# Optimization experiments

Hardware: AMD Instinct MI355X
Metric: run time of the kernel (lower is better)

Reference implementation:

```python
import jax, jax.numpy as jnp
import numpy as np

B, S, D, H, KD = 4, 2048, 640, 10, 64


def setup_inputs() -> dict:
    key = jax.random.key(0)
    k0, k1, k2, k3, k4 = jax.random.split(key, 5)
    x = jax.random.normal(k0, (B, S, D), dtype=jnp.float32)
    # per-head projection weights, stacked over heads: [H, D, KD]
    Wq = jax.random.normal(k1, (H, D, KD), dtype=jnp.float32) * 0.05
    Wk = jax.random.normal(k2, (H, D, KD), dtype=jnp.float32) * 0.05
    Wv = jax.random.normal(k3, (H, D, KD), dtype=jnp.float32) * 0.05
    # output projection: [H*KD, D]
    Wo = jax.random.normal(k4, (H * KD, D), dtype=jnp.float32) * 0.05
    return {"x": x, "Wq": Wq, "Wk": Wk, "Wv": Wv, "Wo": Wo}


def reference(x, Wq, Wk, Wv, Wo):
    # Batched equivalent of the per-head Python loop:
    # each head computes q=x@Wq_h, k=x@Wk_h, v=x@Wv_h, softmax(q k^T / sqrt(KD)) @ v
    q = jnp.einsum("bsd,hdk->bhsk", x, Wq)
    k = jnp.einsum("bsd,hdk->bhsk", x, Wk)
    v = jnp.einsum("bsd,hdk->bhsk", x, Wv)
    scale = 1.0 / jnp.sqrt(jnp.asarray(KD, x.dtype))
    scores = jnp.einsum("bhsk,bhtk->bhst", q, k) * scale  # [B,H,S,S]
    attn = jax.nn.softmax(scores, axis=-1)
    z = jnp.einsum("bhst,bhtk->bhsk", attn, v)  # [B,H,S,KD]
    # concat heads along last axis (head 0 first, matching the loop order)
    z = z.transpose(0, 2, 1, 3).reshape(x.shape[0], x.shape[1], H * KD)
    return jnp.einsum("bsf,fd->bsd", z, Wo)
```

## Files before the change

kernel.cpp:

```cpp
#include <hip/hip_runtime.h>
#include <hip/hip_bf16.h>

#define B_  4
#define S_  2048
#define D_  640
#define H_  10
#define KD_ 64

typedef __attribute__((ext_vector_type(8))) short  short8;
typedef __attribute__((ext_vector_type(4))) short  short4v;
typedef __attribute__((ext_vector_type(4))) float  floatx4;
typedef __attribute__((ext_vector_type(2))) unsigned int uint2v;

static __device__ __forceinline__ short f2bf(float f) {
    union { __hip_bfloat16 h; short s; } u;
    u.h = __float2bfloat16(f);
    return u.s;
}
static __device__ __forceinline__ unsigned int pack2bf(float a, float b) {
    return (unsigned int)(unsigned short)f2bf(a) |
           ((unsigned int)(unsigned short)f2bf(b) << 16);
}

static __device__ __forceinline__ void gload_lds16(const void* gp, void* lp) {
    __builtin_amdgcn_global_load_lds(
        (const __attribute__((address_space(1))) unsigned int*)gp,
        (__attribute__((address_space(3))) unsigned int*)lp, 16, 0, 0);
}

__global__ __launch_bounds__(256) void prep(
        const float* __restrict__ x,
        const float* __restrict__ Wq, const float* __restrict__ Wk,
        const float* __restrict__ Wv, const float* __restrict__ Wo,
        short* __restrict__ xb, short* __restrict__ BigT,
        short* __restrict__ WoT) {
    __shared__ float tile[32][33];
    int bid = blockIdx.x;
    if (bid < 5120) {
        int idx = (bid * 256 + threadIdx.x) * 4;
        float4 v = *(const float4*)(x + idx);
        short4v o;
        o[0] = f2bf(v.x); o[1] = f2bf(v.y); o[2] = f2bf(v.z); o[3] = f2bf(v.w);
        *(short4v*)(xb + idx) = o;
    } else if (bid < 6320) {
        int flat = bid - 5120;
        int bz = flat / 40, rem = flat % 40;
        int by = rem >> 1, bxx = rem & 1;
        int w = bz / 10, h = bz % 10;
        const float* W = ((w == 0) ? Wq : (w == 1) ? Wk : Wv) + h * 640 * 64;
        short* out = BigT + (w * 640 + h * 64) * 640;
        int c0 = bxx * 32;
        int r0 = by * 32;
        int tx = threadIdx.x & 31, ty = threadIdx.x >> 5;
        #pragma unroll
        for (int k = 0; k < 4; ++k)
            tile[ty + 8 * k][tx] = W[(r0 + ty + 8 * k) * 64 + c0 + tx];
        __syncthreads();
        #pragma unroll
        for (int k = 0; k < 4; ++k)
            out[(c0 + ty + 8 * k) * 640 + r0 + tx] = f2bf(tile[tx][ty + 8 * k]);
    } else {
        int flat = bid - 6320;
        int c0 = (flat % 20) * 32;
        int r0 = (flat / 20) * 32;
        int tx = threadIdx.x & 31, ty = threadIdx.x >> 5;
        #pragma unroll
        for (int k = 0; k < 4; ++k)
            tile[ty + 8 * k][tx] = Wo[(r0 + ty + 8 * k) * 640 + c0 + tx];
        __syncthreads();
        #pragma unroll
        for (int k = 0; k < 4; ++k)
            WoT[(c0 + ty + 8 * k) * 640 + r0 + tx] = f2bf(tile[tx][ty + 8 * k]);
    }
}

__global__ __launch_bounds__(256) void qkv_gemm(
        const short* __restrict__ X, const short* __restrict__ BigT,
        short* __restrict__ qb, short* __restrict__ kb, short* __restrict__ vtb) {
    __shared__ __align__(16) short Ab[128][64];
    __shared__ __align__(16) short Bb[128][64];

    int wave = threadIdx.x >> 6;
    int lane = threadIdx.x & 63;
    int lq = lane & 15, quad = lane >> 4;
    int wm = (wave & 1) * 64, wn = (wave >> 1) * 64;
    int tm = blockIdx.x * 128;
    int tn = blockIdx.y * 128;

    int r8 = lane >> 3;
    int sc = ((lane & 7) ^ r8) * 8;
    const short* Asrc = X    + (tm + wave * 32 + r8) * 640 + sc;
    const short* Bsrc = BigT + (tn + wave * 32 + r8) * 640 + sc;

    floatx4 acc[4][4];
    for (int a = 0; a < 4; ++a)
        for (int n = 0; n < 4; ++n)
            acc[a][n] = (floatx4){0.f, 0.f, 0.f, 0.f};

    int swz = lq & 7;
    for (int k0 = 0; k0 < 640; k0 += 64) {
        __syncthreads();
        #pragma unroll
        for (int c = 0; c < 4; ++c) {
            gload_lds16(Asrc + c * 8 * 640 + k0, &Ab[wave * 32 + c * 8][0]);
            gload_lds16(Bsrc + c * 8 * 640 + k0, &Bb[wave * 32 + c * 8][0]);
        }
        __syncthreads();

        #pragma unroll
        for (int ks = 0; ks < 2; ++ks) {
            short8 af[4], bf[4];
            #pragma unroll
            for (int t = 0; t < 4; ++t) {
                af[t] = *(const short8*)(&Ab[wm + t * 16 + lq][((ks * 4 + quad) ^ swz) * 8]);
                bf[t] = *(const short8*)(&Bb[wn + t * 16 + lq][((ks * 4 + quad) ^ swz) * 8]);
            }
            #pragma unroll
            for (int mt = 0; mt < 4; ++mt)
                #pragma unroll
                for (int nt = 0; nt < 4; ++nt)
                    acc[mt][nt] = __builtin_amdgcn_mfma_f32_16x16x32_bf16(
                        af[mt], bf[nt], acc[mt][nt], 0, 0, 0);
        }
    }

    const float qscale = 0.18033688011112042f;
    #pragma unroll
    for (int nt = 0; nt < 4; ++nt) {
        int n_base = tn + wn + nt * 16;
        int w = n_base / 640, rem = n_base % 640;
        int hh = rem / 64, kd = (rem % 64) + lq;
        #pragma unroll
        for (int mt = 0; mt < 4; ++mt) {
            #pragma unroll
            for (int r = 0; r < 4; ++r) {
                int m = tm + wm + mt * 16 + quad * 4 + r;
                int b = m >> 11, s = m & 2047;
                float val = acc[mt][nt][r];
                if (w == 0) {
                    qb[((b * H_ + hh) * S_ + s) * KD_ + kd] = f2bf(val * qscale);
                } else if (w == 1) {
                    kb[((b * H_ + hh) * S_ + s) * KD_ + kd] = f2bf(val);
                } else {
                    vtb[((b * H_ + hh) * KD_ + kd) * S_ + s] = f2bf(val);
                }
            }
        }
    }
}

__global__ __launch_bounds__(256, 3) void attn(
        const short* __restrict__ qb, const short* __restrict__ kbuf,
        const short* __restrict__ vtb, short* __restrict__ zb) {
    __shared__ __align__(16) short Kbuf[2][64][64];
    __shared__ __align__(16) short Vbuf[2][64][64];
    __shared__ __align__(16) short Pbuf[4][2][16][72];

    int wave = threadIdx.x >> 6;
    int lane = threadIdx.x & 63;
    int lq = lane & 15, quad = lane >> 4;

    int bx = blockIdx.x;
    int xcd = bx & 7, slot = bx >> 3;
    int bh = xcd * 5 + (slot >> 4);
    int qt = slot & 15;
    int b = bh / 10, h = bh % 10;
    int q0 = qt * 128;

    const short* qp = qb + (b * H_ + h) * S_ * KD_;
    const short* kp = kbuf + (b * H_ + h) * S_ * KD_;
    const short* vp = vtb + (b * H_ + h) * KD_ * S_;

    int r8 = lane >> 3;
    int g  = (lane & 7) ^ r8;
    const short* kg0 = kp + (wave * 16 + r8) * 64 + g * 8;
    const short* kg1 = kp + (wave * 16 + 8 + r8) * 64 + g * 8;
    const short* vg0 = vp + (wave * 16 + r8) * (long)S_ + g * 8;
    const short* vg1 = vp + (wave * 16 + 8 + r8) * (long)S_ + g * 8;

    short8 qA0, qA1, qB0, qB1;
    {
        int rowA = q0 + wave * 32 + lq;
        qA0 = *(const short8*)(qp + rowA * 64 + quad * 8);
        qA1 = *(const short8*)(qp + rowA * 64 + 32 + quad * 8);
        qB0 = *(const short8*)(qp + (rowA + 16) * 64 + quad * 8);
        qB1 = *(const short8*)(qp + (rowA + 16) * 64 + 32 + quad * 8);
    }

    floatx4 OA[4], OB[4];
    for (int n = 0; n < 4; ++n) {
        OA[n] = (floatx4){0.f, 0.f, 0.f, 0.f};
        OB[n] = (floatx4){0.f, 0.f, 0.f, 0.f};
    }
    float lsA = 0.f, lsB = 0.f;

    gload_lds16(kg0, &Kbuf[0][wave * 16][0]);
    gload_lds16(kg1, &Kbuf[0][wave * 16 + 8][0]);
    gload_lds16(vg0, &Vbuf[0][wave * 16][0]);
    gload_lds16(vg1, &Vbuf[0][wave * 16 + 8][0]);

    int p = 0;
    int sw = lq & 7;

    for (int t0 = 0; t0 < S_; t0 += 64) {
        __syncthreads();

        if (t0 + 64 < S_) {
            int pn = p ^ 1;
            gload_lds16(kg0 + (t0 + 64) * 64, &Kbuf[pn][wave * 16][0]);
            gload_lds16(kg1 + (t0 + 64) * 64, &Kbuf[pn][wave * 16 + 8][0]);
            gload_lds16(vg0 + (t0 + 64),      &Vbuf[pn][wave * 16][0]);
            gload_lds16(vg1 + (t0 + 64),      &Vbuf[pn][wave * 16 + 8][0]);
        }

        const short* Kb = &Kbuf[p][0][0];
        const short* Vb = &Vbuf[p][0][0];

        floatx4 sTA[4], sTB[4];
        #pragma unroll
        for (int kblk = 0; kblk < 4; ++kblk) {
            const short* krow = Kb + (kblk * 16 + lq) * 64;
            short8 bk0 = *(const short8*)(krow + (quad ^ sw) * 8);
            short8 bk1 = *(const short8*)(krow + ((quad + 4) ^ sw) * 8);
            floatx4 zA = (floatx4){0.f, 0.f, 0.f, 0.f};
            zA = __builtin_amdgcn_mfma_f32_16x16x32_bf16(bk0, qA0, zA, 0, 0, 0);
            sTA[kblk] = __builtin_amdgcn_mfma_f32_16x16x32_bf16(bk1, qA1, zA, 0, 0, 0);
            floatx4 zB = (floatx4){0.f, 0.f, 0.f, 0.f};
            zB = __builtin_amdgcn_mfma_f32_16x16x32_bf16(bk0, qB0, zB, 0, 0, 0);
            sTB[kblk] = __builtin_amdgcn_mfma_f32_16x16x32_bf16(bk1, qB1, zB, 0, 0, 0);
        }

        #pragma unroll
        for (int kblk = 0; kblk < 4; ++kblk) {
            float a0 = __builtin_amdgcn_exp2f(sTA[kblk][0]);
            float a1 = __builtin_amdgcn_exp2f(sTA[kblk][1]);
            float a2 = __builtin_amdgcn_exp2f(sTA[kblk][2]);
            float a3 = __builtin_amdgcn_exp2f(sTA[kblk][3]);
            lsA += (a0 + a1) + (a2 + a3);
            uint2v wa; wa[0] = pack2bf(a0, a1); wa[1] = pack2bf(a2, a3);
            *(uint2v*)(&Pbuf[wave][0][lq][kblk * 16 + quad * 4]) = wa;
            float b0 = __builtin_amdgcn_exp2f(sTB[kblk][0]);
            float b1 = __builtin_amdgcn_exp2f(sTB[kblk][1]);
            float b2 = __builtin_amdgcn_exp2f(sTB[kblk][2]);
            float b3 = __builtin_amdgcn_exp2f(sTB[kblk][3]);
            lsB += (b0 + b1) + (b2 + b3);
            uint2v wb; wb[0] = pack2bf(b0, b1); wb[1] = pack2bf(b2, b3);
            *(uint2v*)(&Pbuf[wave][1][lq][kblk * 16 + quad * 4]) = wb;
        }

        #pragma unroll
        for (int ts = 0; ts < 2; ++ts) {
            short8 pfA = *(const short8*)(&Pbuf[wave][0][lq][ts * 32 + quad * 8]);
            short8 pfB = *(const short8*)(&Pbuf[wave][1][lq][ts * 32 + quad * 8]);
            #pragma unroll
            for (int db = 0; db < 4; ++db) {
                const short* vrow = Vb + (db * 16 + lq) * 64;
                short8 bv = *(const short8*)(vrow + ((ts * 4 + quad) ^ sw) * 8);
                OA[db] = __builtin_amdgcn_mfma_f32_16x16x32_bf16(bv, pfA, OA[db], 0, 0, 0);
                OB[db] = __builtin_amdgcn_mfma_f32_16x16x32_bf16(bv, pfB, OB[db], 0, 0, 0);
            }
        }

        p ^= 1;
    }

    lsA += __shfl_xor(lsA, 16);
    lsA += __shfl_xor(lsA, 32);
    lsB += __shfl_xor(lsB, 16);
    lsB += __shfl_xor(lsB, 32);
    float invA = 1.0f / lsA, invB = 1.0f / lsB;

    int sA = q0 + wave * 32 + lq;
    int sB = sA + 16;
    short* zrA = zb + (b * S_ + sA) * 640 + h * 64;
    short* zrB = zb + (b * S_ + sB) * 640 + h * 64;
    #pragma unroll
    for (int db = 0; db < 4; ++db) {
        uint2v za, zv;
        za[0] = pack2bf(OA[db][0] * invA, OA[db][1] * invA);
        za[1] = pack2bf(OA[db][2] * invA, OA[db][3] * invA);
        *(uint2v*)(zrA + db * 16 + quad * 4) = za;
        zv[0] = pack2bf(OB[db][0] * invB, OB[db][1] * invB);
        zv[1] = pack2bf(OB[db][2] * invB, OB[db][3] * invB);
        *(uint2v*)(zrB + db * 16 + quad * 4) = zv;
    }
}

__global__ __launch_bounds__(256) void out_gemm(
        const short* __restrict__ Z, const short* __restrict__ WoT,
        float* __restrict__ out) {
    __shared__ __align__(16) short Ab[128][64];
    __shared__ __align__(16) short Bb[128][64];

    int wave = threadIdx.x >> 6;
    int lane = threadIdx.x & 63;
    int lq = lane & 15, quad = lane >> 4;
    int wm = (wave & 1) * 64, wn = (wave >> 1) * 64;
    int tm = blockIdx.x * 128;
    int tn = blockIdx.y * 128;

    int r8 = lane >> 3;
    int sc = ((lane & 7) ^ r8) * 8;
    const short* Asrc = Z   + (tm + wave * 32 + r8) * 640 + sc;
    const short* Bsrc = WoT + (tn + wave * 32 + r8) * 640 + sc;

    floatx4 acc[4][4];
    for (int a = 0; a < 4; ++a)
        for (int n = 0; n < 4; ++n)
            acc[a][n] = (floatx4){0.f, 0.f, 0.f, 0.f};

    int swz = lq & 7;
    for (int k0 = 0; k0 < 640; k0 += 64) {
        __syncthreads();
        #pragma unroll
        for (int c = 0; c < 4; ++c) {
            gload_lds16(Asrc + c * 8 * 640 + k0, &Ab[wave * 32 + c * 8][0]);
            gload_lds16(Bsrc + c * 8 * 640 + k0, &Bb[wave * 32 + c * 8][0]);
        }
        __syncthreads();

        #pragma unroll
        for (int ks = 0; ks < 2; ++ks) {
            short8 af[4], bf[4];
            #pragma unroll
            for (int t = 0; t < 4; ++t) {
                af[t] = *(const short8*)(&Ab[wm + t * 16 + lq][((ks * 4 + quad) ^ swz) * 8]);
                bf[t] = *(const short8*)(&Bb[wn + t * 16 + lq][((ks * 4 + quad) ^ swz) * 8]);
            }
            #pragma unroll
            for (int mt = 0; mt < 4; ++mt)
                #pragma unroll
                for (int nt = 0; nt < 4; ++nt)
                    acc[mt][nt] = __builtin_amdgcn_mfma_f32_16x16x32_bf16(
                        af[mt], bf[nt], acc[mt][nt], 0, 0, 0);
        }
    }

    #pragma unroll
    for (int mt = 0; mt < 4; ++mt) {
        #pragma unroll
        for (int nt = 0; nt < 4; ++nt) {
            #pragma unroll
            for (int r = 0; r < 4; ++r) {
                int m = tm + wm + mt * 16 + quad * 4 + r;
                out[m * 640 + tn + wn + nt * 16 + lq] = acc[mt][nt][r];
            }
        }
    }
}

extern "C" void kernel_launch(void* const* d_in, const int* in_sizes, int n_in,
                              void* d_out, int out_size, void* d_ws, size_t ws_size,
                              hipStream_t stream) {
    const float* x  = (const float*)d_in[0];
    const float* Wq = (const float*)d_in[1];
    const float* Wk = (const float*)d_in[2];
    const float* Wv = (const float*)d_in[3];
    const float* Wo = (const float*)d_in[4];
    float* out = (float*)d_out;

    char* ws = (char*)d_ws;
    short* BigT = (short*)(ws);
    short* WoT  = (short*)(ws + 2457600);
    short* xb   = (short*)(ws + 3276800);
    short* qb   = (short*)(ws + 13762560);
    short* kb   = (short*)(ws + 24248320);
    short* vtb  = (short*)(ws + 34734080);
    short* zb   = (short*)(ws + 45219840);

    prep<<<dim3(6720), dim3(256), 0, stream>>>(x, Wq, Wk, Wv, Wo, xb, BigT, WoT);
    qkv_gemm<<<dim3(64, 15), dim3(256), 0, stream>>>(xb, BigT, qb, kb, vtb);
    attn<<<dim3(640), dim3(256), 0, stream>>>(qb, kb, vtb, zb);
    out_gemm<<<dim3(64, 5), dim3(256), 0, stream>>>(zb, WoT, out);
}
```

Before: 199.7 us.

## Compute softmax row sums with MFMA, fast bf16 rounding, transposed V store path

The softmax denominator is now accumulated by an extra MFMA that multiplies a vector of bf16 ones by the P fragments, which removes the per-element VALU adds and the final cross-lane shuffles. It also sums the bf16-rounded P values, so the denominator matches the numerator. The library float-to-bf16 conversion is replaced by an inline round-to-nearest-even bit trick, which drops NaN handling. The QKV GEMM splits Q/K blocks from V blocks, and the V branch swaps the MFMA operands so each lane holds consecutive kd values for the transposed V store. The cost is two extra MFMAs per tile in attention and duplicated GEMM code.

```diff
diff --git a/kernel.cpp b/kernel.cpp
--- a/kernel.cpp
+++ b/kernel.cpp
@@ -12,14 +12,16 @@
 typedef __attribute__((ext_vector_type(4))) float  floatx4;
 typedef __attribute__((ext_vector_type(2))) unsigned int uint2v;
 
-static __device__ __forceinline__ short f2bf(float f) {
-    union { __hip_bfloat16 h; short s; } u;
-    u.h = __float2bfloat16(f);
-    return u.s;
+static __device__ __forceinline__ short f2bf_fast(float f) {
+    unsigned int u = __float_as_uint(f);
+    u += 0x7fffu + ((u >> 16) & 1u);
+    return (short)(u >> 16);
 }
 static __device__ __forceinline__ unsigned int pack2bf(float a, float b) {
-    return (unsigned int)(unsigned short)f2bf(a) |
-           ((unsigned int)(unsigned short)f2bf(b) << 16);
+    unsigned int ua = __float_as_uint(a), ub = __float_as_uint(b);
+    ua += 0x7fffu + ((ua >> 16) & 1u);
+    ub += 0x7fffu + ((ub >> 16) & 1u);
+    return (ua >> 16) | (ub & 0xffff0000u);
 }
 
 static __device__ __forceinline__ void gload_lds16(const void* gp, void* lp) {
@@ -39,9 +41,10 @@
     if (bid < 5120) {
         int idx = (bid * 256 + threadIdx.x) * 4;
         float4 v = *(const float4*)(x + idx);
-        short4v o;
-        o[0] = f2bf(v.x); o[1] = f2bf(v.y); o[2] = f2bf(v.z); o[3] = f2bf(v.w);
-        *(short4v*)(xb + idx) = o;
+        uint2v o;
+        o[0] = pack2bf(v.x, v.y);
+        o[1] = pack2bf(v.z, v.w);
+        *(uint2v*)(xb + idx) = o;
     } else if (bid < 6320) {
         int flat = bid - 5120;
         int bz = flat / 40, rem = flat % 40;
@@ -58,7 +61,7 @@
         __syncthreads();
         #pragma unroll
         for (int k = 0; k < 4; ++k)
-            out[(c0 + ty + 8 * k) * 640 + r0 + tx] = f2bf(tile[tx][ty + 8 * k]);
+            out[(c0 + ty + 8 * k) * 640 + r0 + tx] = f2bf_fast(tile[tx][ty + 8 * k]);
     } else {
         int flat = bid - 6320;
         int c0 = (flat % 20) * 32;
@@ -70,7 +73,7 @@
         __syncthreads();
         #pragma unroll
         for (int k = 0; k < 4; ++k)
-            WoT[(c0 + ty + 8 * k) * 640 + r0 + tx] = f2bf(tile[tx][ty + 8 * k]);
+            WoT[(c0 + ty + 8 * k) * 640 + r0 + tx] = f2bf_fast(tile[tx][ty + 8 * k]);
     }
 }
 
@@ -98,51 +101,88 @@
             acc[a][n] = (floatx4){0.f, 0.f, 0.f, 0.f};
 
     int swz = lq & 7;
-    for (int k0 = 0; k0 < 640; k0 += 64) {
-        __syncthreads();
-        #pragma unroll
-        for (int c = 0; c < 4; ++c) {
-            gload_lds16(Asrc + c * 8 * 640 + k0, &Ab[wave * 32 + c * 8][0]);
-            gload_lds16(Bsrc + c * 8 * 640 + k0, &Bb[wave * 32 + c * 8][0]);
-        }
-        __syncthreads();
-
-        #pragma unroll
-        for (int ks = 0; ks < 2; ++ks) {
-            short8 af[4], bf[4];
-            #pragma unroll
-            for (int t = 0; t < 4; ++t) {
-                af[t] = *(const short8*)(&Ab[wm + t * 16 + lq][((ks * 4 + quad) ^ swz) * 8]);
-                bf[t] = *(const short8*)(&Bb[wn + t * 16 + lq][((ks * 4 + quad) ^ swz) * 8]);
-            }
-            #pragma unroll
-            for (int mt = 0; mt < 4; ++mt)
+
+    if (tn < 1280) {
+        for (int k0 = 0; k0 < 640; k0 += 64) {
+            __syncthreads();
+            #pragma unroll
+            for (int c = 0; c < 4; ++c) {
+                gload_lds16(Asrc + c * 8 * 640 + k0, &Ab[wave * 32 + c * 8][0]);
+                gload_lds16(Bsrc + c * 8 * 640 + k0, &Bb[wave * 32 + c * 8][0]);
+            }
+            __syncthreads();
+            #pragma unroll
+            for (int ks = 0; ks < 2; ++ks) {
+                short8 af[4], bf[4];
+                #pragma unroll
+                for (int t = 0; t < 4; ++t) {
+                    af[t] = *(const short8*)(&Ab[wm + t * 16 + lq][((ks * 4 + quad) ^ swz) * 8]);
+                    bf[t] = *(const short8*)(&Bb[wn + t * 16 + lq][((ks * 4 + quad) ^ swz) * 8]);
+                }
+                #pragma unroll
+                for (int mt = 0; mt < 4; ++mt)
+                    #pragma unroll
+                    for (int nt = 0; nt < 4; ++nt)
+                        acc[mt][nt] = __builtin_amdgcn_mfma_f32_16x16x32_bf16(
+                            af[mt], bf[nt], acc[mt][nt], 0, 0, 0);
+            }
+        }
+        const float qscale = 0.18033688011112042f;
+        short* dst = (tn < 640) ? qb : kb;
+        float scale = (tn < 640) ? qscale : 1.0f;
+        #pragma unroll
+        for (int nt = 0; nt < 4; ++nt) {
+            int rem = (tn + wn + nt * 16) % 640;
+            int hh = rem / 64, kd = (rem % 64) + lq;
+            #pragma unroll
+            for (int mt = 0; mt < 4; ++mt) {
+                #pragma unroll
+                for (int r = 0; r < 4; ++r) {
+                    int m = tm + wm + mt * 16 + quad * 4 + r;
+                    int b = m >> 11, s = m & 2047;
+                    dst[((b * H_ + hh) * S_ + s) * KD_ + kd] =
+                        f2bf_fast(acc[mt][nt][r] * scale);
+                }
+            }
+        }
+    } else {
+        for (int k0 = 0; k0 < 640; k0 += 64) {
+            __syncthreads();
+            #pragma unroll
+            for (int c = 0; c < 4; ++c) {
+                gload_lds16(Asrc + c * 8 * 640 + k0, &Ab[wave * 32 + c * 8][0]);
+                gload_lds16(Bsrc + c * 8 * 640 + k0, &Bb[wave * 32 + c * 8][0]);
+            }
+            __syncthreads();
+            #pragma unroll
+            for (int ks = 0; ks < 2; ++ks) {
+                short8 af[4], bf[4];
+                #pragma unroll
+                for (int t = 0; t < 4; ++t) {
+                    af[t] = *(const short8*)(&Ab[wm + t * 16 + lq][((ks * 4 + quad) ^ swz) * 8]);
+                    bf[t] = *(const short8*)(&Bb[wn + t * 16 + lq][((ks * 4 + quad) ^ swz) * 8]);
+                }
                 #pragma unroll
                 for (int nt = 0; nt < 4; ++nt)
-                    acc[mt][nt] = __builtin_amdgcn_mfma_f32_16x16x32_bf16(
-                        af[mt], bf[nt], acc[mt][nt], 0, 0, 0);
-        }
-    }
-
-    const float qscale = 0.18033688011112042f;
-    #pragma unroll
-    for (int nt = 0; nt < 4; ++nt) {
-        int n_base = tn + wn + nt * 16;
-        int w = n_base / 640, rem = n_base % 640;
-        int hh = rem / 64, kd = (rem % 64) + lq;
-        #pragma unroll
-        for (int mt = 0; mt < 4; ++mt) {
-            #pragma unroll
-            for (int r = 0; r < 4; ++r) {
-                int m = tm + wm + mt * 16 + quad * 4 + r;
+                    #pragma unroll
+                    for (int mt = 0; mt < 4; ++mt)
+                        acc[nt][mt] = __builtin_amdgcn_mfma_f32_16x16x32_bf16(
+                            bf[nt], af[mt], acc[nt][mt], 0, 0, 0);
+            }
+        }
+        #pragma unroll
+        for (int nt = 0; nt < 4; ++nt) {
+            int rem = (tn + wn + nt * 16) - 1280;
+            int hh = rem / 64;
+            int kd0 = (rem % 64) + quad * 4;
+            #pragma unroll
+            for (int mt = 0; mt < 4; ++mt) {
+                int m = tm + wm + mt * 16 + lq;
                 int b = m >> 11, s = m & 2047;
-                float val = acc[mt][nt][r];
-                if (w == 0) {
-                    qb[((b * H_ + hh) * S_ + s) * KD_ + kd] = f2bf(val * qscale);
-                } else if (w == 1) {
-                    kb[((b * H_ + hh) * S_ + s) * KD_ + kd] = f2bf(val);
-                } else {
-                    vtb[((b * H_ + hh) * KD_ + kd) * S_ + s] = f2bf(val);
+                #pragma unroll
+                for (int r = 0; r < 4; ++r) {
+                    vtb[((b * H_ + hh) * KD_ + kd0 + r) * S_ + s] =
+                        f2bf_fast(acc[nt][mt][r]);
                 }
             }
         }
@@ -187,12 +227,17 @@
         qB1 = *(const short8*)(qp + (rowA + 16) * 64 + 32 + quad * 8);
     }
 
+    short8 ones;
+    #pragma unroll
+    for (int i = 0; i < 8; ++i) ones[i] = (short)0x3F80;
+
     floatx4 OA[4], OB[4];
     for (int n = 0; n < 4; ++n) {
         OA[n] = (floatx4){0.f, 0.f, 0.f, 0.f};
         OB[n] = (floatx4){0.f, 0.f, 0.f, 0.f};
     }
-    float lsA = 0.f, lsB = 0.f;
+    floatx4 lsvA = (floatx4){0.f, 0.f, 0.f, 0.f};
+    floatx4 lsvB = (floatx4){0.f, 0.f, 0.f, 0.f};
 
     gload_lds16(kg0, &Kbuf[0][wave * 16][0]);
     gload_lds16(kg1, &Kbuf[0][wave * 16 + 8][0]);
@@ -232,19 +277,17 @@
 
         #pragma unroll
         for (int kblk = 0; kblk < 4; ++kblk) {
-            float a0 = __builtin_amdgcn_exp2f(sTA[kblk][0]);
-            float a1 = __builtin_amdgcn_exp2f(sTA[kblk][1]);
-            float a2 = __builtin_amdgcn_exp2f(sTA[kblk][2]);
-            float a3 = __builtin_amdgcn_exp2f(sTA[kblk][3]);
-            lsA += (a0 + a1) + (a2 + a3);
-            uint2v wa; wa[0] = pack2bf(a0, a1); wa[1] = pack2bf(a2, a3);
+            uint2v wa;
+            wa[0] = pack2bf(__builtin_amdgcn_exp2f(sTA[kblk][0]),
+                            __builtin_amdgcn_exp2f(sTA[kblk][1]));
+            wa[1] = pack2bf(__builtin_amdgcn_exp2f(sTA[kblk][2]),
+                            __builtin_amdgcn_exp2f(sTA[kblk][3]));
             *(uint2v*)(&Pbuf[wave][0][lq][kblk * 16 + quad * 4]) = wa;
-            float b0 = __builtin_amdgcn_exp2f(sTB[kblk][0]);
-            float b1 = __builtin_amdgcn_exp2f(sTB[kblk][1]);
-            float b2 = __builtin_amdgcn_exp2f(sTB[kblk][2]);
-            float b3 = __builtin_amdgcn_exp2f(sTB[kblk][3]);
-            lsB += (b0 + b1) + (b2 + b3);
-            uint2v wb; wb[0] = pack2bf(b0, b1); wb[1] = pack2bf(b2, b3);
+            uint2v wb;
+            wb[0] = pack2bf(__builtin_amdgcn_exp2f(sTB[kblk][0]),
+                            __builtin_amdgcn_exp2f(sTB[kblk][1]));
+            wb[1] = pack2bf(__builtin_amdgcn_exp2f(sTB[kblk][2]),
+                            __builtin_amdgcn_exp2f(sTB[kblk][3]));
             *(uint2v*)(&Pbuf[wave][1][lq][kblk * 16 + quad * 4]) = wb;
         }
 
@@ -252,6 +295,8 @@
         for (int ts = 0; ts < 2; ++ts) {
             short8 pfA = *(const short8*)(&Pbuf[wave][0][lq][ts * 32 + quad * 8]);
             short8 pfB = *(const short8*)(&Pbuf[wave][1][lq][ts * 32 + quad * 8]);
+            lsvA = __builtin_amdgcn_mfma_f32_16x16x32_bf16(ones, pfA, lsvA, 0, 0, 0);
+            lsvB = __builtin_amdgcn_mfma_f32_16x16x32_bf16(ones, pfB, lsvB, 0, 0, 0);
             #pragma unroll
             for (int db = 0; db < 4; ++db) {
                 const short* vrow = Vb + (db * 16 + lq) * 64;
@@ -264,11 +309,8 @@
         p ^= 1;
     }
 
-    lsA += __shfl_xor(lsA, 16);
-    lsA += __shfl_xor(lsA, 32);
-    lsB += __shfl_xor(lsB, 16);
-    lsB += __shfl_xor(lsB, 32);
-    float invA = 1.0f / lsA, invB = 1.0f / lsB;
+    float invA = 1.0f / lsvA[0];
+    float invB = 1.0f / lsvB[0];
 
     int sA = q0 + wave * 32 + lq;
     int sB = sA + 16;
```

Result: faster. 190.4 us (-4.7%).
